# Performance work log

Measured on AMD Instinct MI355X. Metric: run time of the kernel, lower is better.

Reference implementation:

```python
import jax, jax.numpy as jnp
import numpy as np

B, NQ, NK, D, DV = 16, 2048, 2048, 128, 128


def setup_inputs() -> dict:
    key = jax.random.key(0)
    kq, kk, kv, kl = jax.random.split(key, 4)
    return {
        "queries": jax.random.normal(kq, (B, NQ, D), dtype=jnp.float32),
        "keys": jax.random.normal(kk, (B, NK, D), dtype=jnp.float32),
        "values": jax.random.normal(kv, (B, NK, DV), dtype=jnp.float32),
        "valid_lens": jax.random.randint(kl, (B,), 1, NK + 1, dtype=jnp.int32),
    }


def reference(queries, keys, values, valid_lens):
    d = queries.shape[-1]
    # scores: [B, NQ, NK]
    scores = jnp.einsum("bqd,bkd->bqk", queries, keys) / jnp.sqrt(jnp.float32(d))
    # mask positions >= valid_len with -1e6 (matches sequence_mask semantics)
    key_pos = jnp.arange(scores.shape[-1], dtype=jnp.int32)  # [NK]
    mask = key_pos[None, None, :] < valid_lens[:, None, None]  # [B,1,NK] -> broadcast over queries
    scores = jnp.where(mask, scores, jnp.float32(-1000000.0))
    attn = jax.nn.softmax(scores, axis=-1)
    # dropout p=0.0 -> identity
    return jnp.einsum("bqk,bkv->bqv", attn, values)
```

## Files before the change

kernel.cpp:

```cpp
#include <hip/hip_runtime.h>


#define B_   16
#define NQ_  2048
#define NK_  2048
#define D_   128
#define DV_  128
#define NTASK_ 512

typedef unsigned short ushort;
typedef __attribute__((ext_vector_type(4))) float          f32x4;
typedef __attribute__((ext_vector_type(8))) __bf16         bf16x8;
typedef __attribute__((ext_vector_type(8))) unsigned short ushort8v;
typedef __attribute__((ext_vector_type(4))) unsigned int   uint4v;

#ifdef __has_builtin
#if __has_builtin(__builtin_amdgcn_cvt_pk_bf16_f32)
#define HAVE_CVT_PK_BF16 1
#endif
#endif

__device__ __forceinline__ ushort f2bf(float f) {
    unsigned u = __builtin_bit_cast(unsigned, f);
    return (ushort)((u + 0x8000u) >> 16);
}
__device__ __forceinline__ float bf2f(ushort h) {
    unsigned u = ((unsigned)h) << 16;
    return __builtin_bit_cast(float, u);
}
__device__ __forceinline__ unsigned f2bf2(float a, float b) {
#ifdef HAVE_CVT_PK_BF16
    auto t = __builtin_amdgcn_cvt_pk_bf16_f32(a, b);
    return __builtin_bit_cast(unsigned, t);
#else
    return (unsigned)f2bf(a) | ((unsigned)f2bf(b) << 16);
#endif
}

__device__ __forceinline__ void gl_lds16(const ushort* g, ushort* l) {
    __builtin_amdgcn_global_load_lds(
        (const __attribute__((address_space(1))) void*)g,
        (__attribute__((address_space(3))) void*)l, 16, 0, 0);
}

__global__ void make_schedule(const int* __restrict__ vlen, int* __restrict__ task) {
    __shared__ int s[16];
    int tid = threadIdx.x;
    if (tid < 16) {
        int my = vlen[tid];
        int rank = 0;
        for (int o = 0; o < 16; ++o) {
            int vo = vlen[o];
            if (vo > my || (vo == my && o < tid)) ++rank;
        }
        s[rank] = tid;
    }
    __syncthreads();
    for (int e = tid; e < NTASK_; e += 64) {
        int half = e >> 8;
        int r    = e & 255;
        int p    = r >> 5;
        int qt   = r & 31;
        int b    = half ? s[15 - p] : s[p];
        task[e]  = b | (qt << 8);
    }
}

__global__ __launch_bounds__(256) void convert_kv(
    const float* __restrict__ K, const float* __restrict__ V,
    const int* __restrict__ vlen, ushort* __restrict__ Kb, ushort* __restrict__ Vtb)
{
    const int id = blockIdx.x;
    const int b  = id & 15, kt = id >> 4;
    if (kt >= ((vlen[b] + 63) >> 6)) return;
    const int tid = threadIdx.x;
    const float* gK = K + ((size_t)b * NK_ + kt * 64) * D_;
    const float* gV = V + ((size_t)b * NK_ + kt * 64) * DV_;
    ushort* tK = Kb  + ((size_t)b * 32 + kt) * 8192;
    ushort* tV = Vtb + ((size_t)b * 32 + kt) * 8192;

    #pragma unroll
    for (int i = 0; i < 4; ++i) {
        int u = i * 256 + tid;
        int key = u >> 4, d8 = u & 15;
        const float* p = gK + key * D_ + d8 * 8;
        f32x4 a0 = *(const f32x4*)p;
        f32x4 a1 = *(const f32x4*)(p + 4);
        uint4v w;
        w[0] = f2bf2(a0[0], a0[1]); w[1] = f2bf2(a0[2], a0[3]);
        w[2] = f2bf2(a1[0], a1[1]); w[3] = f2bf2(a1[2], a1[3]);
        *(uint4v*)&tK[key * 128 + ((d8 ^ (key & 7)) << 3)] = w;
    }
    #pragma unroll
    for (int i = 0; i < 4; ++i) {
        int u = i * 256 + tid;
        int dv = u & 127, kg = u >> 7;
        const float* vp = gV + (size_t)(kg * 8) * DV_ + dv;
        float v[8];
        #pragma unroll
        for (int j = 0; j < 8; ++j) v[j] = vp[(size_t)j * DV_];
        uint4v w;
        w[0] = f2bf2(v[0], v[1]); w[1] = f2bf2(v[2], v[3]);
        w[2] = f2bf2(v[4], v[5]); w[3] = f2bf2(v[6], v[7]);
        *(uint4v*)&tV[dv * 64 + ((kg ^ (dv & 7)) << 3)] = w;
    }
}

__global__ __launch_bounds__(256, 2) void attn_fwd(
    const float* __restrict__ Q, const int* __restrict__ vlen,
    const int* __restrict__ task, const ushort* __restrict__ Kb,
    const ushort* __restrict__ Vtb, float* __restrict__ Out)
{
    __shared__ ushort KVbuf[2][16384];
    __shared__ ushort Pb[4][32][40];
    __shared__ float  lsh[2][64];
    float* Osh = (float*)&KVbuf[0][0];

    const int tid  = threadIdx.x;
    const int w    = tid >> 6;
    const int wq   = w >> 1;
    const int wk   = w & 1;
    const int L    = tid & 63;
    const int col  = L & 15;
    const int quad = L >> 4;

    const int tk    = task[blockIdx.x];
    const int b     = tk & 255;
    const int qbase = (tk >> 8) * 64;
    const int vl    = vlen[b];
    const int ntiles = (vl + 63) >> 6;

    const float qscale = 0.12751743f;
    bf16x8 qf[2][4];
    #pragma unroll
    for (int q16 = 0; q16 < 2; ++q16) {
        const int qrow = qbase + wq * 32 + q16 * 16 + col;
        const float* gQ = Q + ((size_t)b * NQ_ + qrow) * D_;
        #pragma unroll
        for (int c = 0; c < 4; ++c) {
            const float* p = gQ + c * 32 + quad * 8;
            f32x4 a0 = *(const f32x4*)p;
            f32x4 a1 = *(const f32x4*)(p + 4);
            uint4v us;
            us[0] = f2bf2(a0[0] * qscale, a0[1] * qscale);
            us[1] = f2bf2(a0[2] * qscale, a0[3] * qscale);
            us[2] = f2bf2(a1[0] * qscale, a1[1] * qscale);
            us[3] = f2bf2(a1[2] * qscale, a1[3] * qscale);
            qf[q16][c] = __builtin_bit_cast(bf16x8, us);
        }
    }

    f32x4 o[2][8];
    #pragma unroll
    for (int q16 = 0; q16 < 2; ++q16)
        #pragma unroll
        for (int d = 0; d < 8; ++d) o[q16][d] = (f32x4){0.f, 0.f, 0.f, 0.f};
    float l_run[2][4] = {{0.f,0.f,0.f,0.f},{0.f,0.f,0.f,0.f}};

    const ushort* tKb = Kb  + (size_t)b * 32 * 8192;
    const ushort* tVb = Vtb + (size_t)b * 32 * 8192;

    #define ISSUE_DMA(KT, BUF)                                               \
        do {                                                                 \
            const ushort* gk = tKb + (size_t)(KT) * 8192;                    \
            const ushort* gv = tVb + (size_t)(KT) * 8192;                    \
            _Pragma("unroll")                                                \
            for (int i = 0; i < 4; ++i) {                                    \
                int off = (i * 256 + tid) * 8;                               \
                gl_lds16(gk + off, &KVbuf[BUF][off]);                        \
                gl_lds16(gv + off, &KVbuf[BUF][8192 + off]);                 \
            }                                                                \
        } while (0)

    ISSUE_DMA(0, 0);

    for (int kt = 0; kt < ntiles; ++kt) {
        const int buf = kt & 1;
        __syncthreads();
        if (kt + 1 < ntiles) ISSUE_DMA(kt + 1, buf ^ 1);

        const ushort* Kt = &KVbuf[buf][0];
        const ushort* Vt = &KVbuf[buf][8192];
        const int k0 = kt * 64;

        f32x4 s[2][2];
        #pragma unroll
        for (int kc = 0; kc < 2; ++kc) {
            const int key = wk * 32 + kc * 16 + col;
            bf16x8 kb[4];
            #pragma unroll
            for (int c = 0; c < 4; ++c)
                kb[c] = __builtin_bit_cast(bf16x8, *(const ushort8v*)
                    &Kt[key * 128 + (((c * 4 + quad) ^ (col & 7)) << 3)]);
            #pragma unroll
            for (int q16 = 0; q16 < 2; ++q16) {
                f32x4 acc = (f32x4){0.f, 0.f, 0.f, 0.f};
                #pragma unroll
                for (int c = 0; c < 4; ++c)
                    acc = __builtin_amdgcn_mfma_f32_16x16x32_bf16(qf[q16][c], kb[c], acc, 0, 0, 0);
                s[q16][kc] = acc;
            }
        }

        if (k0 + 64 > vl) {
            #pragma unroll
            for (int kc = 0; kc < 2; ++kc)
                if (k0 + wk * 32 + kc * 16 + col >= vl) {
                    s[0][kc] = (f32x4){-1e30f,-1e30f,-1e30f,-1e30f};
                    s[1][kc] = (f32x4){-1e30f,-1e30f,-1e30f,-1e30f};
                }
        }

        #pragma unroll
        for (int q16 = 0; q16 < 2; ++q16)
            #pragma unroll
            for (int kc = 0; kc < 2; ++kc)
                #pragma unroll
                for (int r = 0; r < 4; ++r) {
                    ushort pb = f2bf(exp2f(s[q16][kc][r]));
                    Pb[w][q16 * 16 + quad * 4 + r][kc * 16 + col] = pb;
                    l_run[q16][r] += bf2f(pb);
                }


        bf16x8 pa[2];
        #pragma unroll
        for (int q16 = 0; q16 < 2; ++q16)
            pa[q16] = __builtin_bit_cast(bf16x8,
                *(const ushort8v*)&Pb[w][q16 * 16 + col][quad * 8]);
        #pragma unroll
        for (int dvc = 0; dvc < 8; ++dvc) {
            const int dv = dvc * 16 + col;
            bf16x8 vb = __builtin_bit_cast(bf16x8, *(const ushort8v*)
                &Vt[dv * 64 + (((wk * 4 + quad) ^ (col & 7)) << 3)]);
            #pragma unroll
            for (int q16 = 0; q16 < 2; ++q16)
                o[q16][dvc] = __builtin_amdgcn_mfma_f32_16x16x32_bf16(pa[q16], vb, o[q16][dvc], 0, 0, 0);
        }
    }
    #undef ISSUE_DMA

    #pragma unroll
    for (int off = 1; off < 16; off <<= 1)
        #pragma unroll
        for (int q16 = 0; q16 < 2; ++q16)
            #pragma unroll
            for (int r = 0; r < 4; ++r)
                l_run[q16][r] += __shfl_xor(l_run[q16][r], off, 64);

    __syncthreads();

    if (col == 0) {
        #pragma unroll
        for (int q16 = 0; q16 < 2; ++q16)
            #pragma unroll
            for (int r = 0; r < 4; ++r)
                lsh[wk][wq * 32 + q16 * 16 + quad * 4 + r] = l_run[q16][r];
    }
    #pragma unroll
    for (int q16 = 0; q16 < 2; ++q16)
        #pragma unroll
        for (int dvc = 0; dvc < 8; ++dvc)
            #pragma unroll
            for (int r = 0; r < 4; ++r)
                Osh[wk * 8192 + (wq * 32 + q16 * 16 + quad * 4 + r) * 128 + dvc * 16 + col]
                    = o[q16][dvc][r];
    __syncthreads();

    float* gO = Out + ((size_t)b * NQ_ + qbase) * DV_;
    #pragma unroll
    for (int i = 0; i < 8; ++i) {
        int idx = i * 256 + tid;
        int row = idx >> 5;
        int dq  = idx & 31;
        f32x4 a0 = *(const f32x4*)&Osh[row * 128 + dq * 4];
        f32x4 a1 = *(const f32x4*)&Osh[8192 + row * 128 + dq * 4];
        float linv = 1.0f / (lsh[0][row] + lsh[1][row]);
        f32x4 r = (a0 + a1) * linv;
        *(f32x4*)&gO[(size_t)row * DV_ + dq * 4] = r;
    }
}

extern "C" void kernel_launch(void* const* d_in, const int* in_sizes, int n_in,
                              void* d_out, int out_size, void* d_ws, size_t ws_size,
                              hipStream_t stream) {
    const float* Q  = (const float*)d_in[0];
    const float* K  = (const float*)d_in[1];
    const float* V  = (const float*)d_in[2];
    const int*   vl = (const int*)d_in[3];
    float* out = (float*)d_out;

    char* ws = (char*)d_ws;
    int* task = (int*)ws;
    ushort* Kbuf = (ushort*)(ws + 4096);
    ushort* Vbuf = Kbuf + (size_t)B_ * 32 * 8192;

    make_schedule<<<1, 64, 0, stream>>>(vl, task);
    convert_kv<<<dim3(512, 1, 1), dim3(256, 1, 1), 0, stream>>>(K, V, vl, Kbuf, Vbuf);
    attn_fwd<<<dim3(NTASK_, 1, 1), dim3(256, 1, 1), 0, stream>>>(
        Q, vl, task, Kbuf, Vbuf, out);
}
```

Measured before the change: 138.1 us.

## Load V fragments directly from global, halve LDS, drop task scheduler

V tiles are no longer staged through LDS. Each wave reads its V fragments straight from global memory into registers, which halves the shared buffer and allows three blocks per SM instead of two. The schedule kernel that sorted batches by valid length is removed, so blocks map to batches round-robin and one launch disappears, at the cost of less balanced work per batch. The epilogue now has the wk=0 waves combine partial outputs from registers and write global memory directly, but those writes are strided and less coalesced, and global V loads may add latency on the critical path.

```diff
diff --git a/kernel.cpp b/kernel.cpp
--- a/kernel.cpp
+++ b/kernel.cpp
@@ -41,29 +41,6 @@
     __builtin_amdgcn_global_load_lds(
         (const __attribute__((address_space(1))) void*)g,
         (__attribute__((address_space(3))) void*)l, 16, 0, 0);
-}
-
-__global__ void make_schedule(const int* __restrict__ vlen, int* __restrict__ task) {
-    __shared__ int s[16];
-    int tid = threadIdx.x;
-    if (tid < 16) {
-        int my = vlen[tid];
-        int rank = 0;
-        for (int o = 0; o < 16; ++o) {
-            int vo = vlen[o];
-            if (vo > my || (vo == my && o < tid)) ++rank;
-        }
-        s[rank] = tid;
-    }
-    __syncthreads();
-    for (int e = tid; e < NTASK_; e += 64) {
-        int half = e >> 8;
-        int r    = e & 255;
-        int p    = r >> 5;
-        int qt   = r & 31;
-        int b    = half ? s[15 - p] : s[p];
-        task[e]  = b | (qt << 8);
-    }
 }
 
 __global__ __launch_bounds__(256) void convert_kv(
@@ -102,19 +79,19 @@
         uint4v w;
         w[0] = f2bf2(v[0], v[1]); w[1] = f2bf2(v[2], v[3]);
         w[2] = f2bf2(v[4], v[5]); w[3] = f2bf2(v[6], v[7]);
-        *(uint4v*)&tV[dv * 64 + ((kg ^ (dv & 7)) << 3)] = w;
-    }
-}
-
-__global__ __launch_bounds__(256, 2) void attn_fwd(
+        *(uint4v*)&tV[dv * 64 + kg * 8] = w;
+    }
+}
+
+__global__ __launch_bounds__(256, 3) void attn_fwd(
     const float* __restrict__ Q, const int* __restrict__ vlen,
-    const int* __restrict__ task, const ushort* __restrict__ Kb,
-    const ushort* __restrict__ Vtb, float* __restrict__ Out)
+    const ushort* __restrict__ Kb, const ushort* __restrict__ Vtb,
+    float* __restrict__ Out)
 {
-    __shared__ ushort KVbuf[2][16384];
+    __shared__ ushort Kbuf[2][8192];
     __shared__ ushort Pb[4][32][40];
     __shared__ float  lsh[2][64];
-    float* Osh = (float*)&KVbuf[0][0];
+    float* Osh = (float*)&Kbuf[0][0];
 
     const int tid  = threadIdx.x;
     const int w    = tid >> 6;
@@ -124,9 +101,8 @@
     const int col  = L & 15;
     const int quad = L >> 4;
 
-    const int tk    = task[blockIdx.x];
-    const int b     = tk & 255;
-    const int qbase = (tk >> 8) * 64;
+    const int b     = blockIdx.x & 15;
+    const int qbase = (blockIdx.x >> 4) * 64;
     const int vl    = vlen[b];
     const int ntiles = (vl + 63) >> 6;
 
@@ -163,12 +139,10 @@
     #define ISSUE_DMA(KT, BUF)                                               \
         do {                                                                 \
             const ushort* gk = tKb + (size_t)(KT) * 8192;                    \
-            const ushort* gv = tVb + (size_t)(KT) * 8192;                    \
             _Pragma("unroll")                                                \
             for (int i = 0; i < 4; ++i) {                                    \
                 int off = (i * 256 + tid) * 8;                               \
-                gl_lds16(gk + off, &KVbuf[BUF][off]);                        \
-                gl_lds16(gv + off, &KVbuf[BUF][8192 + off]);                 \
+                gl_lds16(gk + off, &Kbuf[BUF][off]);                         \
             }                                                                \
         } while (0)
 
@@ -177,10 +151,20 @@
     for (int kt = 0; kt < ntiles; ++kt) {
         const int buf = kt & 1;
         __syncthreads();
+
+        bf16x8 vb[8];
+        {
+            const ushort* gVt = tVb + (size_t)kt * 8192;
+            #pragma unroll
+            for (int dvc = 0; dvc < 8; ++dvc) {
+                const int dv = dvc * 16 + col;
+                vb[dvc] = __builtin_bit_cast(bf16x8,
+                    *(const ushort8v*)&gVt[dv * 64 + (wk * 4 + quad) * 8]);
+            }
+        }
         if (kt + 1 < ntiles) ISSUE_DMA(kt + 1, buf ^ 1);
 
-        const ushort* Kt = &KVbuf[buf][0];
-        const ushort* Vt = &KVbuf[buf][8192];
+        const ushort* Kt = &Kbuf[buf][0];
         const int k0 = kt * 64;
 
         f32x4 s[2][2];
@@ -230,12 +214,9 @@
                 *(const ushort8v*)&Pb[w][q16 * 16 + col][quad * 8]);
         #pragma unroll
         for (int dvc = 0; dvc < 8; ++dvc) {
-            const int dv = dvc * 16 + col;
-            bf16x8 vb = __builtin_bit_cast(bf16x8, *(const ushort8v*)
-                &Vt[dv * 64 + (((wk * 4 + quad) ^ (col & 7)) << 3)]);
             #pragma unroll
             for (int q16 = 0; q16 < 2; ++q16)
-                o[q16][dvc] = __builtin_amdgcn_mfma_f32_16x16x32_bf16(pa[q16], vb, o[q16][dvc], 0, 0, 0);
+                o[q16][dvc] = __builtin_amdgcn_mfma_f32_16x16x32_bf16(pa[q16], vb[dvc], o[q16][dvc], 0, 0, 0);
         }
     }
     #undef ISSUE_DMA
@@ -257,27 +238,33 @@
             for (int r = 0; r < 4; ++r)
                 lsh[wk][wq * 32 + q16 * 16 + quad * 4 + r] = l_run[q16][r];
     }
-    #pragma unroll
-    for (int q16 = 0; q16 < 2; ++q16)
-        #pragma unroll
-        for (int dvc = 0; dvc < 8; ++dvc)
-            #pragma unroll
-            for (int r = 0; r < 4; ++r)
-                Osh[wk * 8192 + (wq * 32 + q16 * 16 + quad * 4 + r) * 128 + dvc * 16 + col]
-                    = o[q16][dvc][r];
+    if (wk == 1) {
+        #pragma unroll
+        for (int q16 = 0; q16 < 2; ++q16)
+            #pragma unroll
+            for (int dvc = 0; dvc < 8; ++dvc)
+                #pragma unroll
+                for (int r = 0; r < 4; ++r)
+                    Osh[(wq * 32 + q16 * 16 + quad * 4 + r) * 128 + dvc * 16 + col]
+                        = o[q16][dvc][r];
+    }
     __syncthreads();
 
-    float* gO = Out + ((size_t)b * NQ_ + qbase) * DV_;
-    #pragma unroll
-    for (int i = 0; i < 8; ++i) {
-        int idx = i * 256 + tid;
-        int row = idx >> 5;
-        int dq  = idx & 31;
-        f32x4 a0 = *(const f32x4*)&Osh[row * 128 + dq * 4];
-        f32x4 a1 = *(const f32x4*)&Osh[8192 + row * 128 + dq * 4];
-        float linv = 1.0f / (lsh[0][row] + lsh[1][row]);
-        f32x4 r = (a0 + a1) * linv;
-        *(f32x4*)&gO[(size_t)row * DV_ + dq * 4] = r;
+    if (wk == 0) {
+        float* gO = Out + ((size_t)b * NQ_ + qbase) * DV_;
+        #pragma unroll
+        for (int q16 = 0; q16 < 2; ++q16) {
+            #pragma unroll
+            for (int r = 0; r < 4; ++r) {
+                const int row = wq * 32 + q16 * 16 + quad * 4 + r;
+                const float linv = 1.0f / (l_run[q16][r] + lsh[1][row]);
+                #pragma unroll
+                for (int dvc = 0; dvc < 8; ++dvc) {
+                    float v = (o[q16][dvc][r] + Osh[row * 128 + dvc * 16 + col]) * linv;
+                    gO[(size_t)row * DV_ + dvc * 16 + col] = v;
+                }
+            }
+        }
     }
 }
 
@@ -290,13 +277,10 @@
     const int*   vl = (const int*)d_in[3];
     float* out = (float*)d_out;
 
-    char* ws = (char*)d_ws;
-    int* task = (int*)ws;
-    ushort* Kbuf = (ushort*)(ws + 4096);
+    ushort* Kbuf = (ushort*)d_ws;
     ushort* Vbuf = Kbuf + (size_t)B_ * 32 * 8192;
 
-    make_schedule<<<1, 64, 0, stream>>>(vl, task);
     convert_kv<<<dim3(512, 1, 1), dim3(256, 1, 1), 0, stream>>>(K, V, vl, Kbuf, Vbuf);
     attn_fwd<<<dim3(NTASK_, 1, 1), dim3(256, 1, 1), 0, stream>>>(
-        Q, vl, task, Kbuf, Vbuf, out);
-}
+        Q, vl, Kbuf, Vbuf, out);
+}
```

After: 215.2 us. 55.9% more time.
